# Kernel optimization log

Hardware: AMD Instinct MI355X
Metric: run time of the kernel (lower is better)

The kernel has to match this reference:

```python
import jax, jax.numpy as jnp
import numpy as np

E, B, L, H1, H2, C = 8, 4096, 512, 1024, 512, 40


def setup_inputs() -> dict:
    key = jax.random.key(0)
    ks = jax.random.split(key, 9)
    return {
        "x_s": jax.random.normal(ks[0], (B, L), jnp.float32),
        "x_p": jax.random.normal(ks[1], (B, L), jnp.float32),
        "W1": jax.random.normal(ks[2], (E, 2 * L, H1), jnp.float32) / np.sqrt(2 * L).astype(np.float32),
        "b1": jax.random.normal(ks[3], (E, H1), jnp.float32) * 0.01,
        "W2": jax.random.normal(ks[4], (E, H1, H2), jnp.float32) / np.sqrt(H1).astype(np.float32),
        "b2": jax.random.normal(ks[5], (E, H2), jnp.float32) * 0.01,
        "W3": jax.random.normal(ks[6], (E, H2, C), jnp.float32) / np.sqrt(H2).astype(np.float32),
        "b3": jax.random.normal(ks[7], (E, C), jnp.float32) * 0.01,
        "sub_module_label": jax.random.randint(ks[8], (B,), 0, E, dtype=jnp.int32),
        "sub_id": 0,
    }


def reference(x_s, x_p, W1, b1, W2, b2, W3, b3, sub_module_label, sub_id):
    # Encoders (EEGNet/SCN/DCN) abstracted as identity: x_s / x_p are latent features.
    # Cls_HEAD.forward: x = cat([x_p, x_s], dim=1); per-sample routed 3-layer ELU MLP head.
    # Dropout is identity in eval mode.
    x = jnp.concatenate([x_p, x_s], axis=1)                      # [B, 2L]
    h = jax.nn.elu(jnp.einsum('bi,eih->ebh', x, W1) + b1[:, None, :])   # [E, B, H1]
    h = jax.nn.elu(jnp.einsum('ebh,ehk->ebk', h, W2) + b2[:, None, :])  # [E, B, H2]
    out_all = jnp.einsum('ebk,ekc->ebc', h, W3) + b3[:, None, :]        # [E, B, C]
    # select each sample's routed expert output
    bidx = jnp.arange(x.shape[0])
    return out_all[sub_module_label, bidx]                       # [B, C]
```

## Files before the change

kernel.cpp:

```cpp
#include <hip/hip_runtime.h>
#include <hip/hip_bf16.h>
#include <math.h>

#define En   8
#define Bn   4096
#define Ln   512
#define K1n  1024
#define H1n  1024
#define H2n  512
#define Cn   40
#define NP3  48

typedef unsigned short u16;
typedef __attribute__((ext_vector_type(8))) short bf16x8;
typedef __attribute__((ext_vector_type(4))) float f32x4;

__device__ __forceinline__ u16 f2b(float f) {
    union { float f; unsigned int u; } v; v.f = f;
    unsigned int r = v.u + 0x7FFF + ((v.u >> 16) & 1);
    return (u16)(r >> 16);
}

__device__ __forceinline__ void g2l16(const void* g, void* l) {
    __builtin_amdgcn_global_load_lds(
        (const __attribute__((address_space(1))) unsigned int*)(unsigned long long)g,
        (__attribute__((address_space(3))) unsigned int*)(unsigned int)(unsigned long long)l,
        16, 0, 0);
}

#define PB_X0   1
#define PB_X    256
#define PB_W1   2048
#define PB_W2   1024
#define PB_W3   128
#define PB_OUT  64
#define PB_TOT  (PB_X0 + PB_X + PB_W1 + PB_W2 + PB_W3 + PB_OUT)

__device__ __forceinline__ void wtrans64(
    const float* __restrict__ Wsrc, u16* __restrict__ Wdst,
    int K, int N, int k0, int n0, int tid, float* sm )
{
    #pragma unroll
    for (int s = 0; s < 4; s++) {
        int idx = tid + s * 256;
        int kk = idx >> 4, c4 = (idx & 15) * 4;
        float4 v = *(const float4*)&Wsrc[(size_t)(k0 + kk) * N + n0 + c4];
        float* row = sm + kk * 65 + c4;
        row[0] = v.x; row[1] = v.y; row[2] = v.z; row[3] = v.w;
    }
    __syncthreads();
    #pragma unroll
    for (int s = 0; s < 4; s++) {
        int idx = tid + s * 256;
        int nn = idx >> 4, kc = (idx & 15) * 4;
        ushort4 o = make_ushort4(f2b(sm[(kc + 0) * 65 + nn]), f2b(sm[(kc + 1) * 65 + nn]),
                                 f2b(sm[(kc + 2) * 65 + nn]), f2b(sm[(kc + 3) * 65 + nn]));
        *(ushort4*)&Wdst[(size_t)(n0 + nn) * K + k0 + kc] = o;
    }
}

__global__ __launch_bounds__(256) void prep_kernel(
    const float* __restrict__ xs, const float* __restrict__ xp,
    const float* __restrict__ W1, const float* __restrict__ W2,
    const float* __restrict__ W3, const float* __restrict__ b3,
    const int* __restrict__ label,
    int* __restrict__ meta, int* __restrict__ perm,
    u16* __restrict__ Xb, u16* __restrict__ W1t,
    u16* __restrict__ W2t, u16* __restrict__ W3t,
    float* __restrict__ out)
{
    __shared__ __align__(16) float sm[64 * 65];
    const int bid = blockIdx.x;
    const int tid = threadIdx.x;

    if (bid == 0) {
        int* cnt = (int*)sm;
        int* off = cnt + En;
        if (tid < En) cnt[tid] = 0;
        __syncthreads();
        for (int b = tid; b < Bn; b += 256) atomicAdd(&cnt[label[b]], 1);
        __syncthreads();
        if (tid == 0) {
            int run = 0;
            for (int e = 0; e < En; e++) { off[e] = run; run += cnt[e]; }
            off[En] = run;
        }
        __syncthreads();
        if (tid < En) cnt[tid] = off[tid];
        __syncthreads();
        for (int b = tid; b < Bn; b += 256) {
            int e = label[b];
            perm[atomicAdd(&cnt[e], 1)] = b;
        }
        if (tid <= En) meta[tid] = off[tid];
    } else if (bid < PB_X0 + PB_X) {
        int r0 = (bid - PB_X0) * 16;
        #pragma unroll 4
        for (int s = 0; s < 16; s++) {
            int r = r0 + s;
            int k = tid * 4;
            const float* src = (k < Ln) ? (xp + (size_t)r * Ln + k)
                                        : (xs + (size_t)r * Ln + (k - Ln));
            float4 v = *(const float4*)src;
            *(ushort4*)&Xb[(size_t)r * K1n + k] =
                make_ushort4(f2b(v.x), f2b(v.y), f2b(v.z), f2b(v.w));
        }
    } else if (bid < PB_X0 + PB_X + PB_W1) {
        int b = bid - (PB_X0 + PB_X);
        int e = b >> 8, rem = b & 255;
        int k0 = (rem >> 4) * 64, n0 = (rem & 15) * 64;
        wtrans64(W1 + (size_t)e * K1n * H1n, W1t + (size_t)e * H1n * K1n,
                 K1n, H1n, k0, n0, tid, sm);
    } else if (bid < PB_X0 + PB_X + PB_W1 + PB_W2) {
        int b = bid - (PB_X0 + PB_X + PB_W1);
        int e = b >> 7, rem = b & 127;
        int k0 = (rem >> 3) * 64, n0 = (rem & 7) * 64;
        wtrans64(W2 + (size_t)e * H1n * H2n, W2t + (size_t)e * H2n * H1n,
                 H1n, H2n, k0, n0, tid, sm);
    } else if (bid < PB_X0 + PB_X + PB_W1 + PB_W2 + PB_W3) {
        int b = bid - (PB_X0 + PB_X + PB_W1 + PB_W2);
        int e = b >> 4, k0 = (b & 15) * 32;
        const float* src = W3 + (size_t)e * H2n * Cn;
        u16* dst = W3t + (size_t)e * NP3 * H2n;
        float* t = sm;
        #pragma unroll
        for (int s = 0; s < 5; s++) {
            int idx = tid + s * 256;
            int kk = idx / Cn, nn = idx - kk * Cn;
            if (kk < 32) t[kk * 41 + nn] = src[(size_t)(k0 + kk) * Cn + nn];
        }
        __syncthreads();
        #pragma unroll
        for (int s = 0; s < 6; s++) {
            int idx = tid + s * 256;
            int nn = idx >> 5, kk = idx & 31;
            float v = (nn < Cn) ? t[kk * 41 + nn] : 0.f;
            dst[(size_t)nn * H2n + k0 + kk] = f2b(v);
        }
    } else {
        int b = bid - (PB_X0 + PB_X + PB_W1 + PB_W2 + PB_W3);
        int r0 = b * 64;
        #pragma unroll
        for (int s = 0; s < 10; s++) {
            int idx = tid + s * 256;
            int r = r0 + idx / Cn;
            int c = idx - (idx / Cn) * Cn;
            out[(size_t)r * Cn + c] = b3[label[r] * Cn + c];
        }
    }
}

template <int K, int N, bool GATHER, bool FUSE3>
__global__ __launch_bounds__(256) void mfma_gemm(
    const u16* __restrict__ A, const u16* __restrict__ Wt,
    const float* __restrict__ bias, const int* __restrict__ meta,
    const int* __restrict__ perm, u16* __restrict__ outb,
    const u16* __restrict__ Wt3, float* __restrict__ outf)
{
    constexpr int TM = 64, TN = 64, BK = 32;
    constexpr int T = K / BK;
    __shared__ __align__(16) u16 SM[8192];

    const int tid = threadIdx.x;
    const int bx = blockIdx.x;

    int expert = -1, row0 = 0, rowmax = 0, acc_t = 0;
    int prev = meta[0];
    #pragma unroll
    for (int e = 0; e < En; e++) {
        int nxt = meta[e + 1];
        int c = nxt - prev;
        int t = (c + TM - 1) / TM;
        if (expert < 0 && bx < acc_t + t) {
            expert = e; row0 = prev + (bx - acc_t) * TM; rowmax = nxt - 1;
        }
        acc_t += t; prev = nxt;
    }
    if (expert < 0) return;

    const int col0 = blockIdx.y * TN;
    const u16* Wexp = Wt + (size_t)expert * N * K;

    const int lane = tid & 63;
    const int wid = tid >> 6;
    const int wm = (wid & 1) * 32;
    const int wn = (wid >> 1) * 32;
    const int l15 = lane & 15;
    const int lq = lane >> 4;

    const int rl = tid >> 2, cch = tid & 3;
    const int kq = cch ^ (rl & 3);
    int rg = row0 + rl; if (rg > rowmax) rg = rowmax;
    if (GATHER) rg = perm[rg];
    const u16* aptr = A + (size_t)rg * K + kq * 8;
    const u16* bptr = Wexp + (size_t)(col0 + rl) * K + kq * 8;
    const int aoff = tid * 8;
    const int boff = 2048 + tid * 8;
    const int ksw = (lq ^ (l15 & 3)) * 8;

    f32x4 acc[2][2];
    #pragma unroll
    for (int i = 0; i < 2; i++)
        #pragma unroll
        for (int j = 0; j < 2; j++) acc[i][j] = (f32x4){0.f, 0.f, 0.f, 0.f};

    g2l16(aptr, &SM[aoff]);
    g2l16(bptr, &SM[boff]);

    for (int t = 0; t < T; t++) {
        __syncthreads();
        const u16* As = &SM[(t & 1) * 4096];
        const u16* Bs = As + 2048;
        if (t + 1 < T) {
            int base = ((t + 1) & 1) * 4096;
            int ko = (t + 1) * BK;
            g2l16(aptr + ko, &SM[base + aoff]);
            g2l16(bptr + ko, &SM[base + boff]);
        }
        bf16x8 af[2], bf[2];
        #pragma unroll
        for (int i = 0; i < 2; i++)
            af[i] = *(const bf16x8*)&As[(wm + i * 16 + l15) * BK + ksw];
        #pragma unroll
        for (int j = 0; j < 2; j++)
            bf[j] = *(const bf16x8*)&Bs[(wn + j * 16 + l15) * BK + ksw];
        #pragma unroll
        for (int i = 0; i < 2; i++)
            #pragma unroll
            for (int j = 0; j < 2; j++)
                acc[i][j] = __builtin_amdgcn_mfma_f32_16x16x32_bf16(
                    af[i], bf[j], acc[i][j], 0, 0, 0);
    }

    if (!FUSE3) {
        #pragma unroll
        for (int i = 0; i < 2; i++) {
            #pragma unroll
            for (int j = 0; j < 2; j++) {
                int col = col0 + wn + j * 16 + l15;
                float bv = bias[expert * N + col];
                #pragma unroll
                for (int r = 0; r < 4; r++) {
                    int grow = row0 + wm + i * 16 + lq * 4 + r;
                    if (grow <= rowmax) {
                        float v = acc[i][j][r] + bv;
                        v = (v > 0.f) ? v : (expf(v) - 1.f);
                        outb[(size_t)grow * N + col] = f2b(v);
                    }
                }
            }
        }
    } else {
        __syncthreads();
        u16* H = &SM[0];
        #pragma unroll
        for (int i = 0; i < 2; i++) {
            #pragma unroll
            for (int j = 0; j < 2; j++) {
                int col = wn + j * 16 + l15;
                float bv = bias[expert * N + col0 + col];
                #pragma unroll
                for (int r = 0; r < 4; r++) {
                    float v = acc[i][j][r] + bv;
                    v = (v > 0.f) ? v : (expf(v) - 1.f);
                    H[(wm + i * 16 + lq * 4 + r) * 72 + col] = f2b(v);
                }
            }
        }
        __syncthreads();
        const int rh = wid * 16;
        f32x4 a3[3];
        #pragma unroll
        for (int j = 0; j < 3; j++) a3[j] = (f32x4){0.f, 0.f, 0.f, 0.f};
        #pragma unroll
        for (int ki = 0; ki < 2; ki++) {
            bf16x8 ha = *(const bf16x8*)&H[(rh + l15) * 72 + ki * 32 + lq * 8];
            #pragma unroll
            for (int j = 0; j < 3; j++) {
                bf16x8 wb = *(const bf16x8*)
                    &Wt3[((size_t)expert * NP3 + j * 16 + l15) * H2n + col0 + ki * 32 + lq * 8];
                a3[j] = __builtin_amdgcn_mfma_f32_16x16x32_bf16(ha, wb, a3[j], 0, 0, 0);
            }
        }
        #pragma unroll
        for (int j = 0; j < 3; j++) {
            int col = j * 16 + l15;
            if (col < Cn) {
                #pragma unroll
                for (int r = 0; r < 4; r++) {
                    int grow = row0 + rh + lq * 4 + r;
                    if (grow <= rowmax)
                        atomicAdd(&outf[(size_t)perm[grow] * Cn + col], a3[j][r]);
                }
            }
        }
    }
}

extern "C" void kernel_launch(void* const* d_in, const int* in_sizes, int n_in,
                              void* d_out, int out_size, void* d_ws, size_t ws_size,
                              hipStream_t stream)
{
    const float* xs = (const float*)d_in[0];
    const float* xp = (const float*)d_in[1];
    const float* W1 = (const float*)d_in[2];
    const float* b1 = (const float*)d_in[3];
    const float* W2 = (const float*)d_in[4];
    const float* b2 = (const float*)d_in[5];
    const float* W3 = (const float*)d_in[6];
    const float* b3 = (const float*)d_in[7];
    const int* label = (const int*)d_in[8];
    float* out = (float*)d_out;

    char* ws = (char*)d_ws;
    int* meta = (int*)ws;
    int* perm = (int*)(ws + 64);
    u16* Xb  = (u16*)(ws + (64 << 10));
    u16* W1t = (u16*)(ws + (64 << 10) + (8  << 20));
    u16* W2t = (u16*)(ws + (64 << 10) + (24 << 20));
    u16* h1b = (u16*)(ws + (64 << 10) + (32 << 20));
    u16* W3t = (u16*)(ws + (64 << 10) + (40 << 20));

    prep_kernel<<<PB_TOT, 256, 0, stream>>>(
        xs, xp, W1, W2, W3, b3, label, meta, perm, Xb, W1t, W2t, W3t, out);

    mfma_gemm<K1n, H1n, true, false><<<dim3(72, 16), 256, 0, stream>>>(
        Xb, W1t, b1, meta, perm, h1b, nullptr, nullptr);

    mfma_gemm<H1n, H2n, false, true><<<dim3(72, 8), 256, 0, stream>>>(
        h1b, W2t, b2, meta, perm, nullptr, W3t, out);
}
```

Before: 173.6 us.

## Move W2/W3 prep into layer-1 GEMM launch and double K tile to 64

Splits the prep kernel so only X conversion, routing and the W1 transpose run before the first GEMM. The W2/W3 transposes and the bias-initialised output are handled by extra blocks appended to the layer-1 GEMM grid, so that work overlaps with GEMM compute. The GEMM K-step grows from 32 to 64 with two loads per thread and an 8-way XOR swizzle, halving the number of barrier/prefetch iterations. This doubles shared memory per block, which may reduce occupancy, and adds a 1D-grid tile decode.

```diff
diff --git a/kernel.cpp b/kernel.cpp
--- a/kernel.cpp
+++ b/kernel.cpp
@@ -10,6 +10,7 @@
 #define H2n  512
 #define Cn   40
 #define NP3  48
+#define NTR  72
 
 typedef unsigned short u16;
 typedef __attribute__((ext_vector_type(8))) short bf16x8;
@@ -27,14 +28,6 @@
         (__attribute__((address_space(3))) unsigned int*)(unsigned int)(unsigned long long)l,
         16, 0, 0);
 }
-
-#define PB_X0   1
-#define PB_X    256
-#define PB_W1   2048
-#define PB_W2   1024
-#define PB_W3   128
-#define PB_OUT  64
-#define PB_TOT  (PB_X0 + PB_X + PB_W1 + PB_W2 + PB_W3 + PB_OUT)
 
 __device__ __forceinline__ void wtrans64(
     const float* __restrict__ Wsrc, u16* __restrict__ Wdst,
@@ -59,15 +52,13 @@
     }
 }
 
-__global__ __launch_bounds__(256) void prep_kernel(
+#define P1_TOT (1 + 256 + 2048)
+
+__global__ __launch_bounds__(256) void prep1_kernel(
     const float* __restrict__ xs, const float* __restrict__ xp,
-    const float* __restrict__ W1, const float* __restrict__ W2,
-    const float* __restrict__ W3, const float* __restrict__ b3,
-    const int* __restrict__ label,
+    const float* __restrict__ W1, const int* __restrict__ label,
     int* __restrict__ meta, int* __restrict__ perm,
-    u16* __restrict__ Xb, u16* __restrict__ W1t,
-    u16* __restrict__ W2t, u16* __restrict__ W3t,
-    float* __restrict__ out)
+    u16* __restrict__ Xb, u16* __restrict__ W1t)
 {
     __shared__ __align__(16) float sm[64 * 65];
     const int bid = blockIdx.x;
@@ -93,8 +84,8 @@
             perm[atomicAdd(&cnt[e], 1)] = b;
         }
         if (tid <= En) meta[tid] = off[tid];
-    } else if (bid < PB_X0 + PB_X) {
-        int r0 = (bid - PB_X0) * 16;
+    } else if (bid < 257) {
+        int r0 = (bid - 1) * 16;
         #pragma unroll 4
         for (int s = 0; s < 16; s++) {
             int r = r0 + s;
@@ -105,64 +96,76 @@
             *(ushort4*)&Xb[(size_t)r * K1n + k] =
                 make_ushort4(f2b(v.x), f2b(v.y), f2b(v.z), f2b(v.w));
         }
-    } else if (bid < PB_X0 + PB_X + PB_W1) {
-        int b = bid - (PB_X0 + PB_X);
+    } else {
+        int b = bid - 257;
         int e = b >> 8, rem = b & 255;
         int k0 = (rem >> 4) * 64, n0 = (rem & 15) * 64;
         wtrans64(W1 + (size_t)e * K1n * H1n, W1t + (size_t)e * H1n * K1n,
                  K1n, H1n, k0, n0, tid, sm);
-    } else if (bid < PB_X0 + PB_X + PB_W1 + PB_W2) {
-        int b = bid - (PB_X0 + PB_X + PB_W1);
-        int e = b >> 7, rem = b & 127;
-        int k0 = (rem >> 3) * 64, n0 = (rem & 7) * 64;
-        wtrans64(W2 + (size_t)e * H1n * H2n, W2t + (size_t)e * H2n * H1n,
-                 H1n, H2n, k0, n0, tid, sm);
-    } else if (bid < PB_X0 + PB_X + PB_W1 + PB_W2 + PB_W3) {
-        int b = bid - (PB_X0 + PB_X + PB_W1 + PB_W2);
-        int e = b >> 4, k0 = (b & 15) * 32;
-        const float* src = W3 + (size_t)e * H2n * Cn;
-        u16* dst = W3t + (size_t)e * NP3 * H2n;
-        float* t = sm;
-        #pragma unroll
-        for (int s = 0; s < 5; s++) {
-            int idx = tid + s * 256;
-            int kk = idx / Cn, nn = idx - kk * Cn;
-            if (kk < 32) t[kk * 41 + nn] = src[(size_t)(k0 + kk) * Cn + nn];
-        }
-        __syncthreads();
-        #pragma unroll
-        for (int s = 0; s < 6; s++) {
-            int idx = tid + s * 256;
-            int nn = idx >> 5, kk = idx & 31;
-            float v = (nn < Cn) ? t[kk * 41 + nn] : 0.f;
-            dst[(size_t)nn * H2n + k0 + kk] = f2b(v);
-        }
-    } else {
-        int b = bid - (PB_X0 + PB_X + PB_W1 + PB_W2 + PB_W3);
-        int r0 = b * 64;
-        #pragma unroll
-        for (int s = 0; s < 10; s++) {
-            int idx = tid + s * 256;
-            int r = r0 + idx / Cn;
-            int c = idx - (idx / Cn) * Cn;
-            out[(size_t)r * Cn + c] = b3[label[r] * Cn + c];
-        }
-    }
-}
-
-template <int K, int N, bool GATHER, bool FUSE3>
+    }
+}
+
+template <int K, int N, bool GATHER, bool FUSE3, bool PREP2>
 __global__ __launch_bounds__(256) void mfma_gemm(
     const u16* __restrict__ A, const u16* __restrict__ Wt,
     const float* __restrict__ bias, const int* __restrict__ meta,
     const int* __restrict__ perm, u16* __restrict__ outb,
-    const u16* __restrict__ Wt3, float* __restrict__ outf)
+    const u16* __restrict__ Wt3, float* __restrict__ outf,
+    const float* __restrict__ W2f, const float* __restrict__ W3f,
+    const float* __restrict__ b3v, const int* __restrict__ labelv,
+    u16* __restrict__ W2t_o, u16* __restrict__ W3t_o)
 {
-    constexpr int TM = 64, TN = 64, BK = 32;
+    constexpr int TM = 64, BK = 64;
     constexpr int T = K / BK;
-    __shared__ __align__(16) u16 SM[8192];
+    constexpr int NTC = N / 64;
+    __shared__ __align__(16) u16 SM[16384];
 
     const int tid = threadIdx.x;
     const int bx = blockIdx.x;
+
+    if (PREP2 && bx >= NTR * NTC) {
+        int jb = bx - NTR * NTC;
+        if (jb < 1024) {
+            int e = jb >> 7, rem = jb & 127;
+            int k0 = (rem >> 3) * 64, n0 = (rem & 7) * 64;
+            wtrans64(W2f + (size_t)e * H1n * H2n, W2t_o + (size_t)e * H2n * H1n,
+                     H1n, H2n, k0, n0, tid, (float*)SM);
+        } else if (jb < 1024 + 128) {
+            int b = jb - 1024;
+            int e = b >> 4, k0 = (b & 15) * 32;
+            const float* src = W3f + (size_t)e * H2n * Cn;
+            u16* dst = W3t_o + (size_t)e * NP3 * H2n;
+            float* t = (float*)SM;
+            #pragma unroll
+            for (int s = 0; s < 5; s++) {
+                int idx = tid + s * 256;
+                int kk = idx / Cn, nn = idx - kk * Cn;
+                if (kk < 32) t[kk * 41 + nn] = src[(size_t)(k0 + kk) * Cn + nn];
+            }
+            __syncthreads();
+            #pragma unroll
+            for (int s = 0; s < 6; s++) {
+                int idx = tid + s * 256;
+                int nn = idx >> 5, kk = idx & 31;
+                float v = (nn < Cn) ? t[kk * 41 + nn] : 0.f;
+                dst[(size_t)nn * H2n + k0 + kk] = f2b(v);
+            }
+        } else {
+            int b = jb - (1024 + 128);
+            int r0 = b * 64;
+            #pragma unroll
+            for (int s = 0; s < 10; s++) {
+                int idx = tid + s * 256;
+                int r = r0 + idx / Cn;
+                int c = idx - (idx / Cn) * Cn;
+                outf[(size_t)r * Cn + c] = b3v[labelv[r] * Cn + c];
+            }
+        }
+        return;
+    }
+
+    const int rt = bx % NTR;
+    const int col0 = (bx / NTR) * 64;
 
     int expert = -1, row0 = 0, rowmax = 0, acc_t = 0;
     int prev = meta[0];
@@ -171,14 +174,13 @@
         int nxt = meta[e + 1];
         int c = nxt - prev;
         int t = (c + TM - 1) / TM;
-        if (expert < 0 && bx < acc_t + t) {
-            expert = e; row0 = prev + (bx - acc_t) * TM; rowmax = nxt - 1;
+        if (expert < 0 && rt < acc_t + t) {
+            expert = e; row0 = prev + (rt - acc_t) * TM; rowmax = nxt - 1;
         }
         acc_t += t; prev = nxt;
     }
     if (expert < 0) return;
 
-    const int col0 = blockIdx.y * TN;
     const u16* Wexp = Wt + (size_t)expert * N * K;
 
     const int lane = tid & 63;
@@ -188,15 +190,21 @@
     const int l15 = lane & 15;
     const int lq = lane >> 4;
 
-    const int rl = tid >> 2, cch = tid & 3;
-    const int kq = cch ^ (rl & 3);
-    int rg = row0 + rl; if (rg > rowmax) rg = rowmax;
-    if (GATHER) rg = perm[rg];
-    const u16* aptr = A + (size_t)rg * K + kq * 8;
-    const u16* bptr = Wexp + (size_t)(col0 + rl) * K + kq * 8;
-    const int aoff = tid * 8;
-    const int boff = 2048 + tid * 8;
-    const int ksw = (lq ^ (l15 & 3)) * 8;
+    const u16* aptr[2]; const u16* bptr[2];
+    int aoff[2], boff[2];
+    #pragma unroll
+    for (int s = 0; s < 2; s++) {
+        int idx = tid + s * 256;
+        int rl = idx >> 3, c = idx & 7;
+        int kq = c ^ (rl & 7);
+        int rg = row0 + rl; if (rg > rowmax) rg = rowmax;
+        if (GATHER) rg = perm[rg];
+        aptr[s] = A + (size_t)rg * K + kq * 8;
+        bptr[s] = Wexp + (size_t)(col0 + rl) * K + kq * 8;
+        aoff[s] = idx * 8;
+        boff[s] = 4096 + idx * 8;
+    }
+    const int csw = l15 & 7;
 
     f32x4 acc[2][2];
     #pragma unroll
@@ -204,32 +212,42 @@
         #pragma unroll
         for (int j = 0; j < 2; j++) acc[i][j] = (f32x4){0.f, 0.f, 0.f, 0.f};
 
-    g2l16(aptr, &SM[aoff]);
-    g2l16(bptr, &SM[boff]);
+    #pragma unroll
+    for (int s = 0; s < 2; s++) {
+        g2l16(aptr[s], &SM[aoff[s]]);
+        g2l16(bptr[s], &SM[boff[s]]);
+    }
 
     for (int t = 0; t < T; t++) {
         __syncthreads();
-        const u16* As = &SM[(t & 1) * 4096];
-        const u16* Bs = As + 2048;
+        const u16* As = &SM[(t & 1) * 8192];
+        const u16* Bs = As + 4096;
         if (t + 1 < T) {
-            int base = ((t + 1) & 1) * 4096;
+            int base = ((t + 1) & 1) * 8192;
             int ko = (t + 1) * BK;
-            g2l16(aptr + ko, &SM[base + aoff]);
-            g2l16(bptr + ko, &SM[base + boff]);
-        }
-        bf16x8 af[2], bf[2];
-        #pragma unroll
-        for (int i = 0; i < 2; i++)
-            af[i] = *(const bf16x8*)&As[(wm + i * 16 + l15) * BK + ksw];
-        #pragma unroll
-        for (int j = 0; j < 2; j++)
-            bf[j] = *(const bf16x8*)&Bs[(wn + j * 16 + l15) * BK + ksw];
-        #pragma unroll
-        for (int i = 0; i < 2; i++)
+            #pragma unroll
+            for (int s = 0; s < 2; s++) {
+                g2l16(aptr[s] + ko, &SM[base + aoff[s]]);
+                g2l16(bptr[s] + ko, &SM[base + boff[s]]);
+            }
+        }
+        #pragma unroll
+        for (int h = 0; h < 2; h++) {
+            const int ksw = ((h * 4 + lq) ^ csw) << 3;
+            bf16x8 af[2], bf[2];
+            #pragma unroll
+            for (int i = 0; i < 2; i++)
+                af[i] = *(const bf16x8*)&As[(wm + i * 16 + l15) * BK + ksw];
             #pragma unroll
             for (int j = 0; j < 2; j++)
-                acc[i][j] = __builtin_amdgcn_mfma_f32_16x16x32_bf16(
-                    af[i], bf[j], acc[i][j], 0, 0, 0);
+                bf[j] = *(const bf16x8*)&Bs[(wn + j * 16 + l15) * BK + ksw];
+            #pragma unroll
+            for (int i = 0; i < 2; i++)
+                #pragma unroll
+                for (int j = 0; j < 2; j++)
+                    acc[i][j] = __builtin_amdgcn_mfma_f32_16x16x32_bf16(
+                        af[i], bf[j], acc[i][j], 0, 0, 0);
+        }
     }
 
     if (!FUSE3) {
@@ -321,12 +339,14 @@
     u16* h1b = (u16*)(ws + (64 << 10) + (32 << 20));
     u16* W3t = (u16*)(ws + (64 << 10) + (40 << 20));
 
-    prep_kernel<<<PB_TOT, 256, 0, stream>>>(
-        xs, xp, W1, W2, W3, b3, label, meta, perm, Xb, W1t, W2t, W3t, out);
-
-    mfma_gemm<K1n, H1n, true, false><<<dim3(72, 16), 256, 0, stream>>>(
-        Xb, W1t, b1, meta, perm, h1b, nullptr, nullptr);
-
-    mfma_gemm<H1n, H2n, false, true><<<dim3(72, 8), 256, 0, stream>>>(
-        h1b, W2t, b2, meta, perm, nullptr, W3t, out);
-}
+    prep1_kernel<<<P1_TOT, 256, 0, stream>>>(
+        xs, xp, W1, label, meta, perm, Xb, W1t);
+
+    mfma_gemm<K1n, H1n, true, false, true><<<72 * 16 + 1216, 256, 0, stream>>>(
+        Xb, W1t, b1, meta, perm, h1b, nullptr, out,
+        W2, W3, b3, label, W2t, W3t);
+
+    mfma_gemm<H1n, H2n, false, true, false><<<72 * 8, 256, 0, stream>>>(
+        h1b, W2t, b2, meta, perm, nullptr, W3t, out,
+        nullptr, nullptr, nullptr, nullptr, nullptr, nullptr);
+}
```

Measured after the change: 172.1 us. About the same (-0.9%).
